# Kernel tuning notes

Hardware: AMD Instinct MI355X
Metric: run time of the kernel (lower is better)

## Reference

```python
import jax, jax.numpy as jnp
import numpy as np

N, D, S, C, H = 65536, 512, 32, 64, 64  # batch, input_size, n_subnets, cols/subnet, hidden
GROUP = 32  # columns per predictor group


def _build_col_ids():
    # 16 groups of 32 cols; interactions = (i,i+1) and (i,i+2) mod 16
    pairs = [(i, (i + 1) % 16) for i in range(16)] + [(i, (i + 2) % 16) for i in range(16)]
    ids = np.array([np.concatenate([np.arange(a * GROUP, (a + 1) * GROUP),
                                    np.arange(b * GROUP, (b + 1) * GROUP)])
                    for a, b in pairs], dtype=np.int32)  # [S, C]
    return jnp.asarray(ids)


def setup_inputs() -> dict:
    key = jax.random.key(0)
    ks = jax.random.split(key, 7)
    scale = 0.05  # keep log_rate inside clamp range most of the time
    return {
        "x": jax.random.normal(ks[0], (N, D), jnp.float32),
        "skip_w": jax.random.normal(ks[1], (D,), jnp.float32) * scale,
        "skip_b": jax.random.normal(ks[2], (1,), jnp.float32) * scale,
        "W1": jax.random.normal(ks[3], (S, C, H), jnp.float32) * scale,
        "b1": jax.random.normal(ks[4], (S, H), jnp.float32) * scale,
        "W2": jax.random.normal(ks[5], (S, H), jnp.float32) * scale,
        "b2": jax.random.normal(ks[6], (S,), jnp.float32) * scale,
        "col_ids": _build_col_ids(),
    }


def reference(x, skip_w, skip_b, W1, b1, W2, b2, col_ids):
    # skip: Linear(D,1) then squeeze -> [N]
    log_rate = x @ skip_w + skip_b[0]
    # fused gather + batched tiny MLP over all S subnets
    xg = x[:, col_ids]                                  # [N, S, C]
    h = jax.nn.relu(jnp.einsum('nsc,sch->nsh', xg, W1) + b1)  # [N, S, H]
    out = jnp.einsum('nsh,sh->ns', h, W2) + b2          # [N, S]
    log_rate = log_rate + out.sum(axis=-1)
    return jnp.clip(log_rate, -20.0, 20.0)
```

## Files before the change

kernel.cpp:

```cpp
#include <hip/hip_runtime.h>
#include <hip/hip_bf16.h>

#define NROWS 65536
#define DCOLS 512

typedef float  f32x4  __attribute__((ext_vector_type(4)));
typedef __bf16 bf16x8 __attribute__((ext_vector_type(8)));

__device__ __forceinline__ unsigned short f2bf(float f) {
    unsigned int u = __builtin_bit_cast(unsigned int, f);
    u += 0x7fffu + ((u >> 16) & 1u);
    return (unsigned short)(u >> 16);
}

__device__ __forceinline__ unsigned int pkbf(float lo, float hi) {
    __hip_bfloat162 t = __float22bfloat162_rn(make_float2(lo, hi));
    unsigned int u;
    __builtin_memcpy(&u, &t, 4);
    return u;
}

__global__ void pack_kernel(const float* __restrict__ W1,
                            const float* __restrict__ b1,
                            const float* __restrict__ W2,
                            unsigned short* __restrict__ w1p,
                            float2* __restrict__ pk) {
    int idx  = blockIdx.x * 256 + threadIdx.x;
    int j    = idx & 7;
    int lane = (idx >> 3) & 63;
    int f    = (idx >> 9) & 7;
    int s    = idx >> 12;
    int kt = f >> 2, nt = f & 3;
    int c = kt * 32 + (lane >> 4) * 8 + j;
    int h = nt * 16 + (lane & 15);
    w1p[idx] = f2bf(W1[(s * 64 + c) * 64 + h]);
    if (idx < 2048) pk[idx] = make_float2(b1[idx], W2[idx]);
}

__launch_bounds__(256, 4)
__global__ void fused_kernel(const float* __restrict__ x,
                             const float* __restrict__ skip_w,
                             const float* __restrict__ skip_b,
                             const float* __restrict__ b2,
                             const unsigned short* __restrict__ w1p,
                             const float2* __restrict__ pk,
                             float* __restrict__ out) {
    __shared__ uint4 w1buf[2][512];

    const int tid  = threadIdx.x;
    const int wave = tid >> 6;
    const int lane = tid & 63;
    const int m    = lane & 15;
    const int q    = lane >> 4;
    const int row0 = blockIdx.x * 64 + wave * 16;

    uint4 afr[16];
    float sp = 0.f;
    const float* xrow = x + (long)(row0 + m) * DCOLS;
#pragma unroll
    for (int g = 0; g < 16; ++g) {
        const float4 sw0 = *(const float4*)(skip_w + g * 32 + q * 8);
        const float4 sw1 = *(const float4*)(skip_w + g * 32 + q * 8 + 4);
        const float4 a0  = *(const float4*)(xrow + g * 32 + q * 8);
        const float4 a1  = *(const float4*)(xrow + g * 32 + q * 8 + 4);
        sp = fmaf(a0.x, sw0.x, fmaf(a0.y, sw0.y, fmaf(a0.z, sw0.z, fmaf(a0.w, sw0.w, sp))));
        sp = fmaf(a1.x, sw1.x, fmaf(a1.y, sw1.y, fmaf(a1.z, sw1.z, fmaf(a1.w, sw1.w, sp))));
        afr[g] = make_uint4(pkbf(a0.x, a0.y), pkbf(a0.z, a0.w),
                            pkbf(a1.x, a1.y), pkbf(a1.z, a1.w));
    }
    float v = sp;
    v += __shfl_xor(v, 16);
    v += __shfl_xor(v, 32);
    const float sf = v;

    float b2s = 0.f;
#pragma unroll
    for (int i = 0; i < 32; ++i) b2s += b2[i];
    const float sb0 = skip_b[0];

    const uint4* wp = (const uint4*)w1p;
    float part[4] = {0.f, 0.f, 0.f, 0.f};

    w1buf[0][tid]       = wp[tid];
    w1buf[0][tid + 256] = wp[tid + 256];
    __syncthreads();

#pragma unroll
    for (int s = 0; s < 32; ++s) {
        const int cb = s & 1, nb = cb ^ 1;
        uint4 pf0, pf1;
        if (s + 1 < 32) {
            pf0 = wp[(s + 1) * 512 + tid];
            pf1 = wp[(s + 1) * 512 + tid + 256];
        }
        const int ga = s & 15;
        const int gb = ((s & 15) + 1 + (s >> 4)) & 15;
        const bf16x8 a0 = __builtin_bit_cast(bf16x8, afr[ga]);
        const bf16x8 a1 = __builtin_bit_cast(bf16x8, afr[gb]);

        f32x4 acc[4];
#pragma unroll
        for (int nt = 0; nt < 4; ++nt) {
            const bf16x8 b0 = __builtin_bit_cast(bf16x8, w1buf[cb][nt * 64 + lane]);
            f32x4 z = {0.f, 0.f, 0.f, 0.f};
            acc[nt] = __builtin_amdgcn_mfma_f32_16x16x32_bf16(a0, b0, z, 0, 0, 0);
        }
#pragma unroll
        for (int nt = 0; nt < 4; ++nt) {
            const bf16x8 b1f = __builtin_bit_cast(bf16x8, w1buf[cb][(4 + nt) * 64 + lane]);
            acc[nt] = __builtin_amdgcn_mfma_f32_16x16x32_bf16(a1, b1f, acc[nt], 0, 0, 0);
        }

#pragma unroll
        for (int nt = 0; nt < 4; ++nt) {
            const float2 bw = pk[s * 64 + nt * 16 + m];
#pragma unroll
            for (int r = 0; r < 4; ++r) {
                float h = acc[nt][r] + bw.x;
                h = fmaxf(h, 0.f);
                part[r] = fmaf(h, bw.y, part[r]);
            }
        }
        __syncthreads();
        if (s + 1 < 32) {
            w1buf[nb][tid]       = pf0;
            w1buf[nb][tid + 256] = pf1;
        }
        __syncthreads();
    }

#pragma unroll
    for (int r = 0; r < 4; ++r) {
        float t = part[r];
        t += __shfl_xor(t, 1);
        t += __shfl_xor(t, 2);
        t += __shfl_xor(t, 4);
        t += __shfl_xor(t, 8);
        const float skipv = __shfl(sf, q * 4 + r);
        float val = t + b2s + sb0 + skipv;
        val = fminf(fmaxf(val, -20.f), 20.f);
        if (m == 0) out[row0 + q * 4 + r] = val;
    }
}

extern "C" void kernel_launch(void* const* d_in, const int* in_sizes, int n_in,
                              void* d_out, int out_size, void* d_ws, size_t ws_size,
                              hipStream_t stream) {
    const float* x      = (const float*)d_in[0];
    const float* skip_w = (const float*)d_in[1];
    const float* skip_b = (const float*)d_in[2];
    const float* W1     = (const float*)d_in[3];
    const float* b1     = (const float*)d_in[4];
    const float* W2     = (const float*)d_in[5];
    const float* b2     = (const float*)d_in[6];

    unsigned short* w1p = (unsigned short*)d_ws;
    float2* pk = (float2*)((char*)d_ws + 262144);

    pack_kernel<<<512, 256, 0, stream>>>(W1, b1, W2, w1p, pk);
    fused_kernel<<<NROWS / 64, 256, 0, stream>>>(x, skip_w, skip_b, b2, w1p, pk,
                                                 (float*)d_out);
}
```

Measured before the change: 239.1 us.

## Stream x loads into the subnet loop and compute skip via MFMA

```diff
diff --git a/kernel.cpp b/kernel.cpp
--- a/kernel.cpp
+++ b/kernel.cpp
@@ -18,6 +18,11 @@
     unsigned int u;
     __builtin_memcpy(&u, &t, 4);
     return u;
+}
+
+__device__ __forceinline__ uint4 packfrag(float4 a0, float4 a1) {
+    return make_uint4(pkbf(a0.x, a0.y), pkbf(a0.z, a0.w),
+                      pkbf(a1.x, a1.y), pkbf(a1.z, a1.w));
 }
 
 __global__ void pack_kernel(const float* __restrict__ W1,
@@ -46,85 +51,100 @@
                              const float2* __restrict__ pk,
                              float* __restrict__ out) {
     __shared__ uint4 w1buf[2][512];
+    __shared__ unsigned int swb[256];
 
     const int tid  = threadIdx.x;
-    const int wave = tid >> 6;
     const int lane = tid & 63;
     const int m    = lane & 15;
     const int q    = lane >> 4;
-    const int row0 = blockIdx.x * 64 + wave * 16;
+    const int row0 = blockIdx.x * 64 + (tid >> 6) * 16;
+
+    const uint4* wp = (const uint4*)w1p;
+    const float* xq = x + (size_t)(row0 + m) * DCOLS + q * 8;
+
+    w1buf[0][tid]       = wp[tid];
+    w1buf[0][tid + 256] = wp[tid + 256];
+    {
+        float2 sw2 = *(const float2*)(skip_w + 2 * tid);
+        swb[tid] = pkbf(sw2.x, sw2.y);
+    }
 
     uint4 afr[16];
-    float sp = 0.f;
-    const float* xrow = x + (long)(row0 + m) * DCOLS;
-#pragma unroll
-    for (int g = 0; g < 16; ++g) {
-        const float4 sw0 = *(const float4*)(skip_w + g * 32 + q * 8);
-        const float4 sw1 = *(const float4*)(skip_w + g * 32 + q * 8 + 4);
-        const float4 a0  = *(const float4*)(xrow + g * 32 + q * 8);
-        const float4 a1  = *(const float4*)(xrow + g * 32 + q * 8 + 4);
-        sp = fmaf(a0.x, sw0.x, fmaf(a0.y, sw0.y, fmaf(a0.z, sw0.z, fmaf(a0.w, sw0.w, sp))));
-        sp = fmaf(a1.x, sw1.x, fmaf(a1.y, sw1.y, fmaf(a1.z, sw1.z, fmaf(a1.w, sw1.w, sp))));
-        afr[g] = make_uint4(pkbf(a0.x, a0.y), pkbf(a0.z, a0.w),
-                            pkbf(a1.x, a1.y), pkbf(a1.z, a1.w));
+    float4 pA[2], pB[2];
+    {
+        float4 t0a = *(const float4*)(xq + 0 * 32), t0b = *(const float4*)(xq + 0 * 32 + 4);
+        float4 t1a = *(const float4*)(xq + 1 * 32), t1b = *(const float4*)(xq + 1 * 32 + 4);
+        pA[0] = *(const float4*)(xq + 2 * 32);
+        pB[0] = *(const float4*)(xq + 2 * 32 + 4);
+        afr[0] = packfrag(t0a, t0b);
+        afr[1] = packfrag(t1a, t1b);
     }
-    float v = sp;
-    v += __shfl_xor(v, 16);
-    v += __shfl_xor(v, 32);
-    const float sf = v;
 
     float b2s = 0.f;
 #pragma unroll
     for (int i = 0; i < 32; ++i) b2s += b2[i];
     const float sb0 = skip_b[0];
 
-    const uint4* wp = (const uint4*)w1p;
     float part[4] = {0.f, 0.f, 0.f, 0.f};
+    f32x4 askip = {0.f, 0.f, 0.f, 0.f};
 
-    w1buf[0][tid]       = wp[tid];
-    w1buf[0][tid + 256] = wp[tid + 256];
     __syncthreads();
 
 #pragma unroll
     for (int s = 0; s < 32; ++s) {
         const int cb = s & 1, nb = cb ^ 1;
-        uint4 pf0, pf1;
+
+        if (s <= 12) {
+            const int gi = s + 3;
+            pA[gi & 1] = *(const float4*)(xq + gi * 32);
+            pB[gi & 1] = *(const float4*)(xq + gi * 32 + 4);
+        }
+        uint4 st0, st1;
         if (s + 1 < 32) {
-            pf0 = wp[(s + 1) * 512 + tid];
-            pf1 = wp[(s + 1) * 512 + tid + 256];
+            st0 = wp[(s + 1) * 512 + tid];
+            st1 = wp[(s + 1) * 512 + tid + 256];
         }
+        if (s <= 13) {
+            const int gp = s + 2;
+            afr[gp] = packfrag(pA[gp & 1], pB[gp & 1]);
+        }
+
         const int ga = s & 15;
         const int gb = ((s & 15) + 1 + (s >> 4)) & 15;
         const bf16x8 a0 = __builtin_bit_cast(bf16x8, afr[ga]);
         const bf16x8 a1 = __builtin_bit_cast(bf16x8, afr[gb]);
 
-        f32x4 acc[4];
-#pragma unroll
-        for (int nt = 0; nt < 4; ++nt) {
-            const bf16x8 b0 = __builtin_bit_cast(bf16x8, w1buf[cb][nt * 64 + lane]);
-            f32x4 z = {0.f, 0.f, 0.f, 0.f};
-            acc[nt] = __builtin_amdgcn_mfma_f32_16x16x32_bf16(a0, b0, z, 0, 0, 0);
-        }
-#pragma unroll
-        for (int nt = 0; nt < 4; ++nt) {
-            const bf16x8 b1f = __builtin_bit_cast(bf16x8, w1buf[cb][(4 + nt) * 64 + lane]);
-            acc[nt] = __builtin_amdgcn_mfma_f32_16x16x32_bf16(a1, b1f, acc[nt], 0, 0, 0);
+        if (s < 16) {
+            uint4 sv = ((const uint4*)swb)[ga * 4 + q];
+            if (m != 0) sv = make_uint4(0u, 0u, 0u, 0u);
+            askip = __builtin_amdgcn_mfma_f32_16x16x32_bf16(
+                a0, __builtin_bit_cast(bf16x8, sv), askip, 0, 0, 0);
         }
 
 #pragma unroll
-        for (int nt = 0; nt < 4; ++nt) {
-            const float2 bw = pk[s * 64 + nt * 16 + m];
+        for (int p = 0; p < 2; ++p) {
+            const float2 bwa = pk[s * 64 + (2 * p) * 16 + m];
+            const float2 bwb = pk[s * 64 + (2 * p + 1) * 16 + m];
+            const bf16x8 b00 = __builtin_bit_cast(bf16x8, w1buf[cb][(2 * p) * 64 + lane]);
+            const bf16x8 b01 = __builtin_bit_cast(bf16x8, w1buf[cb][(2 * p + 1) * 64 + lane]);
+            f32x4 ac0 = {bwa.x, bwa.x, bwa.x, bwa.x};
+            f32x4 ac1 = {bwb.x, bwb.x, bwb.x, bwb.x};
+            ac0 = __builtin_amdgcn_mfma_f32_16x16x32_bf16(a0, b00, ac0, 0, 0, 0);
+            ac1 = __builtin_amdgcn_mfma_f32_16x16x32_bf16(a0, b01, ac1, 0, 0, 0);
+            const bf16x8 b10 = __builtin_bit_cast(bf16x8, w1buf[cb][(4 + 2 * p) * 64 + lane]);
+            const bf16x8 b11 = __builtin_bit_cast(bf16x8, w1buf[cb][(4 + 2 * p + 1) * 64 + lane]);
+            ac0 = __builtin_amdgcn_mfma_f32_16x16x32_bf16(a1, b10, ac0, 0, 0, 0);
+            ac1 = __builtin_amdgcn_mfma_f32_16x16x32_bf16(a1, b11, ac1, 0, 0, 0);
 #pragma unroll
             for (int r = 0; r < 4; ++r) {
-                float h = acc[nt][r] + bw.x;
-                h = fmaxf(h, 0.f);
-                part[r] = fmaf(h, bw.y, part[r]);
+                part[r] = fmaf(fmaxf(ac0[r], 0.f), bwa.y, part[r]);
+                part[r] = fmaf(fmaxf(ac1[r], 0.f), bwb.y, part[r]);
             }
         }
-        __syncthreads();
+
         if (s + 1 < 32) {
-            w1buf[nb][tid]       = pf0;
-            w1buf[nb][tid + 256] = pf1;
+            w1buf[nb][tid]       = st0;
+            w1buf[nb][tid + 256] = st1;
         }
         __syncthreads();
     }
@@ -136,8 +156,7 @@
         t += __shfl_xor(t, 2);
         t += __shfl_xor(t, 4);
         t += __shfl_xor(t, 8);
-        const float skipv = __shfl(sf, q * 4 + r);
-        float val = t + b2s + sb0 + skipv;
+        float val = t + b2s + sb0 + askip[r];
         val = fminf(fmaxf(val, -20.f), 20.f);
         if (m == 0) out[row0 + q * 4 + r] = val;
     }
```

Measured after the change: 226.6 us. -5.2%, faster.

## Use single-wave blocks with two row tiles, direct weight loads, and MFMA skip dot

Applied to the files above, without the earlier changes.

```diff
diff --git a/kernel.cpp b/kernel.cpp
--- a/kernel.cpp
+++ b/kernel.cpp
@@ -20,11 +20,18 @@
     return u;
 }
 
+__device__ __forceinline__ uint4 packfrag(float4 a0, float4 a1) {
+    return make_uint4(pkbf(a0.x, a0.y), pkbf(a0.z, a0.w),
+                      pkbf(a1.x, a1.y), pkbf(a1.z, a1.w));
+}
+
 __global__ void pack_kernel(const float* __restrict__ W1,
                             const float* __restrict__ b1,
                             const float* __restrict__ W2,
+                            const float* __restrict__ skip_w,
                             unsigned short* __restrict__ w1p,
-                            float2* __restrict__ pk) {
+                            float2* __restrict__ pk,
+                            unsigned int* __restrict__ swp) {
     int idx  = blockIdx.x * 256 + threadIdx.x;
     int j    = idx & 7;
     int lane = (idx >> 3) & 63;
@@ -35,112 +42,115 @@
     int h = nt * 16 + (lane & 15);
     w1p[idx] = f2bf(W1[(s * 64 + c) * 64 + h]);
     if (idx < 2048) pk[idx] = make_float2(b1[idx], W2[idx]);
+    if (idx < 256)  swp[idx] = pkbf(skip_w[2 * idx], skip_w[2 * idx + 1]);
 }
 
-__launch_bounds__(256, 4)
+__launch_bounds__(64, 2)
 __global__ void fused_kernel(const float* __restrict__ x,
-                             const float* __restrict__ skip_w,
                              const float* __restrict__ skip_b,
                              const float* __restrict__ b2,
                              const unsigned short* __restrict__ w1p,
                              const float2* __restrict__ pk,
+                             const unsigned int* __restrict__ swp,
                              float* __restrict__ out) {
-    __shared__ uint4 w1buf[2][512];
-
-    const int tid  = threadIdx.x;
-    const int wave = tid >> 6;
-    const int lane = tid & 63;
+    const int lane = threadIdx.x & 63;
     const int m    = lane & 15;
     const int q    = lane >> 4;
-    const int row0 = blockIdx.x * 64 + wave * 16;
+    const int row0 = blockIdx.x * 32;
 
-    uint4 afr[16];
-    float sp = 0.f;
-    const float* xrow = x + (long)(row0 + m) * DCOLS;
-#pragma unroll
-    for (int g = 0; g < 16; ++g) {
-        const float4 sw0 = *(const float4*)(skip_w + g * 32 + q * 8);
-        const float4 sw1 = *(const float4*)(skip_w + g * 32 + q * 8 + 4);
-        const float4 a0  = *(const float4*)(xrow + g * 32 + q * 8);
-        const float4 a1  = *(const float4*)(xrow + g * 32 + q * 8 + 4);
-        sp = fmaf(a0.x, sw0.x, fmaf(a0.y, sw0.y, fmaf(a0.z, sw0.z, fmaf(a0.w, sw0.w, sp))));
-        sp = fmaf(a1.x, sw1.x, fmaf(a1.y, sw1.y, fmaf(a1.z, sw1.z, fmaf(a1.w, sw1.w, sp))));
-        afr[g] = make_uint4(pkbf(a0.x, a0.y), pkbf(a0.z, a0.w),
-                            pkbf(a1.x, a1.y), pkbf(a1.z, a1.w));
+    const uint4* wp   = (const uint4*)w1p;
+    const uint4* swp4 = (const uint4*)swp;
+    const float* xq0 = x + (size_t)(row0 + m) * DCOLS + q * 8;
+    const float* xq1 = xq0 + (size_t)16 * DCOLS;
+
+    uint4 afr[2][16];
+    float4 iA[2][2], iB[2][2], iC[2][2], iD[2][2];
+    {
+        float4 aa = *(const float4*)(xq0 + 0 * 32), ab = *(const float4*)(xq0 + 0 * 32 + 4);
+        float4 ba = *(const float4*)(xq1 + 0 * 32), bb = *(const float4*)(xq1 + 0 * 32 + 4);
+        float4 ca = *(const float4*)(xq0 + 1 * 32), cb = *(const float4*)(xq0 + 1 * 32 + 4);
+        float4 da = *(const float4*)(xq1 + 1 * 32), db = *(const float4*)(xq1 + 1 * 32 + 4);
+        afr[0][0] = packfrag(aa, ab);
+        afr[1][0] = packfrag(ba, bb);
+        afr[0][1] = packfrag(ca, cb);
+        afr[1][1] = packfrag(da, db);
+        iA[0][0] = *(const float4*)(xq0 + 2 * 32); iB[0][0] = *(const float4*)(xq0 + 2 * 32 + 4);
+        iC[0][0] = *(const float4*)(xq1 + 2 * 32); iD[0][0] = *(const float4*)(xq1 + 2 * 32 + 4);
     }
-    float v = sp;
-    v += __shfl_xor(v, 16);
-    v += __shfl_xor(v, 32);
-    const float sf = v;
 
     float b2s = 0.f;
 #pragma unroll
     for (int i = 0; i < 32; ++i) b2s += b2[i];
     const float sb0 = skip_b[0];
 
-    const uint4* wp = (const uint4*)w1p;
-    float part[4] = {0.f, 0.f, 0.f, 0.f};
-
-    w1buf[0][tid]       = wp[tid];
-    w1buf[0][tid + 256] = wp[tid + 256];
-    __syncthreads();
+    float part[2][4] = {{0.f,0.f,0.f,0.f},{0.f,0.f,0.f,0.f}};
+    f32x4 askip[2] = {{0.f,0.f,0.f,0.f},{0.f,0.f,0.f,0.f}};
 
 #pragma unroll
     for (int s = 0; s < 32; ++s) {
-        const int cb = s & 1, nb = cb ^ 1;
-        uint4 pf0, pf1;
-        if (s + 1 < 32) {
-            pf0 = wp[(s + 1) * 512 + tid];
-            pf1 = wp[(s + 1) * 512 + tid + 256];
+        if (s <= 12) {
+            const int gi = s + 3, sl = gi & 1;
+            iA[0][sl] = *(const float4*)(xq0 + gi * 32);
+            iB[0][sl] = *(const float4*)(xq0 + gi * 32 + 4);
+            iC[0][sl] = *(const float4*)(xq1 + gi * 32);
+            iD[0][sl] = *(const float4*)(xq1 + gi * 32 + 4);
         }
+        if (s <= 13) {
+            const int gp = s + 2, sl = gp & 1;
+            afr[0][gp] = packfrag(iA[0][sl], iB[0][sl]);
+            afr[1][gp] = packfrag(iC[0][sl], iD[0][sl]);
+        }
+
+        const uint4* wseg = wp + s * 512;
+        uint4 bf[8];
+#pragma unroll
+        for (int i = 0; i < 8; ++i) bf[i] = wseg[i * 64 + lane];
+
         const int ga = s & 15;
         const int gb = ((s & 15) + 1 + (s >> 4)) & 15;
-        const bf16x8 a0 = __builtin_bit_cast(bf16x8, afr[ga]);
-        const bf16x8 a1 = __builtin_bit_cast(bf16x8, afr[gb]);
 
-        f32x4 acc[4];
+        if (s < 16) {
+            uint4 sv = swp4[ga * 4 + q];
+            if (m != 0) sv = make_uint4(0u, 0u, 0u, 0u);
+            const bf16x8 svb = __builtin_bit_cast(bf16x8, sv);
 #pragma unroll
-        for (int nt = 0; nt < 4; ++nt) {
-            const bf16x8 b0 = __builtin_bit_cast(bf16x8, w1buf[cb][nt * 64 + lane]);
-            f32x4 z = {0.f, 0.f, 0.f, 0.f};
-            acc[nt] = __builtin_amdgcn_mfma_f32_16x16x32_bf16(a0, b0, z, 0, 0, 0);
-        }
-#pragma unroll
-        for (int nt = 0; nt < 4; ++nt) {
-            const bf16x8 b1f = __builtin_bit_cast(bf16x8, w1buf[cb][(4 + nt) * 64 + lane]);
-            acc[nt] = __builtin_amdgcn_mfma_f32_16x16x32_bf16(a1, b1f, acc[nt], 0, 0, 0);
+            for (int mt = 0; mt < 2; ++mt)
+                askip[mt] = __builtin_amdgcn_mfma_f32_16x16x32_bf16(
+                    __builtin_bit_cast(bf16x8, afr[mt][ga]), svb, askip[mt], 0, 0, 0);
         }
 
 #pragma unroll
-        for (int nt = 0; nt < 4; ++nt) {
-            const float2 bw = pk[s * 64 + nt * 16 + m];
+        for (int mt = 0; mt < 2; ++mt) {
+            const bf16x8 a0 = __builtin_bit_cast(bf16x8, afr[mt][ga]);
+            const bf16x8 a1 = __builtin_bit_cast(bf16x8, afr[mt][gb]);
 #pragma unroll
-            for (int r = 0; r < 4; ++r) {
-                float h = acc[nt][r] + bw.x;
-                h = fmaxf(h, 0.f);
-                part[r] = fmaf(h, bw.y, part[r]);
+            for (int nt = 0; nt < 4; ++nt) {
+                const float2 bw = pk[s * 64 + nt * 16 + m];
+                f32x4 ac = {bw.x, bw.x, bw.x, bw.x};
+                ac = __builtin_amdgcn_mfma_f32_16x16x32_bf16(
+                    a0, __builtin_bit_cast(bf16x8, bf[nt]), ac, 0, 0, 0);
+                ac = __builtin_amdgcn_mfma_f32_16x16x32_bf16(
+                    a1, __builtin_bit_cast(bf16x8, bf[4 + nt]), ac, 0, 0, 0);
+#pragma unroll
+                for (int r = 0; r < 4; ++r)
+                    part[mt][r] = fmaf(fmaxf(ac[r], 0.f), bw.y, part[mt][r]);
             }
         }
-        __syncthreads();
-        if (s + 1 < 32) {
-            w1buf[nb][tid]       = pf0;
-            w1buf[nb][tid + 256] = pf1;
-        }
-        __syncthreads();
     }
 
 #pragma unroll
-    for (int r = 0; r < 4; ++r) {
-        float t = part[r];
-        t += __shfl_xor(t, 1);
-        t += __shfl_xor(t, 2);
-        t += __shfl_xor(t, 4);
-        t += __shfl_xor(t, 8);
-        const float skipv = __shfl(sf, q * 4 + r);
-        float val = t + b2s + sb0 + skipv;
-        val = fminf(fmaxf(val, -20.f), 20.f);
-        if (m == 0) out[row0 + q * 4 + r] = val;
-    }
+    for (int mt = 0; mt < 2; ++mt)
+#pragma unroll
+        for (int r = 0; r < 4; ++r) {
+            float t = part[mt][r];
+            t += __shfl_xor(t, 1);
+            t += __shfl_xor(t, 2);
+            t += __shfl_xor(t, 4);
+            t += __shfl_xor(t, 8);
+            float val = t + b2s + sb0 + askip[mt][r];
+            val = fminf(fmaxf(val, -20.f), 20.f);
+            if (m == 0) out[row0 + mt * 16 + q * 4 + r] = val;
+        }
 }
 
 extern "C" void kernel_launch(void* const* d_in, const int* in_sizes, int n_in,
@@ -155,9 +165,10 @@
     const float* b2     = (const float*)d_in[6];
 
     unsigned short* w1p = (unsigned short*)d_ws;
-    float2* pk = (float2*)((char*)d_ws + 262144);
+    float2* pk  = (float2*)((char*)d_ws + 262144);
+    unsigned int* swp = (unsigned int*)((char*)d_ws + 262144 + 16384);
 
-    pack_kernel<<<512, 256, 0, stream>>>(W1, b1, W2, w1p, pk);
-    fused_kernel<<<NROWS / 64, 256, 0, stream>>>(x, skip_w, skip_b, b2, w1p, pk,
-                                                 (float*)d_out);
+    pack_kernel<<<512, 256, 0, stream>>>(W1, b1, W2, skip_w, w1p, pk, swp);
+    fused_kernel<<<NROWS / 32, 64, 0, stream>>>(x, skip_b, b2, w1p, pk, swp,
+                                                (float*)d_out);
 }
```

Result: slower. 858.6 us (+259.1%).
